# Performance work log

Measured on AMD Instinct MI355X. Metric: run time of the kernel, lower is better.

Reference implementation:

```python
import math
import jax, jax.numpy as jnp
import numpy as np

B, C, T, N, H = 4, 512, 2048, 4096, 4


def setup_inputs() -> dict:
    key = jax.random.key(0)
    ks = jax.random.split(key, 6)
    w = lambda k, shape: jax.random.normal(k, shape, dtype=jnp.float32) * 0.02
    return {
        "hidden_states": jax.random.normal(ks[0], (B, C, T), dtype=jnp.float32),
        "codebook_hidden_states": jax.random.normal(ks[1], (N, C), dtype=jnp.float32),
        # Linear weights stored as (in, out) so application is x @ W + b
        "Wq": w(ks[2], (C, C)), "bq": jnp.zeros((C,), jnp.float32),
        "Wk": w(ks[3], (C, C)), "bk": jnp.zeros((C,), jnp.float32),
        "Wv": w(ks[4], (C, C)), "bv": jnp.zeros((C,), jnp.float32),
        "Wp": w(ks[5], (C, H)), "bp": jnp.zeros((H,), jnp.float32),
    }


def reference(hidden_states, codebook_hidden_states, Wq, bq, Wk, bk, Wv, bv, Wp, bp):
    b, c, t = hidden_states.shape
    n = codebook_hidden_states.shape[0]
    h = bp.shape[0]
    d = c // h
    hs = hidden_states.transpose(0, 2, 1)                               # [B,T,C]
    q = (hs @ Wq + bq).reshape(b, t, h, d).transpose(0, 2, 1, 3)        # [B,H,T,d]
    k = (codebook_hidden_states @ Wk + bk).reshape(n, h, d).transpose(1, 0, 2)  # [H,N,d]
    v = codebook_hidden_states @ Wv + bv                                # [N,C]
    cg = hs @ Wp + bp                                                   # [B,T,H] head-pool gates
    scale = 1.0 / math.sqrt(d)
    logits_h = jnp.einsum('bhtd,hnd->bhnt', q, k) * scale               # [B,H,N,T]
    logits = jnp.einsum('bth,bhnt->bnt', cg, logits_h) / math.sqrt(h)   # [B,N,T]
    soft = jax.nn.softmax(logits, axis=1)                               # over codebook axis N
    idx = jnp.argmax(soft, axis=1)                                      # [B,T]
    hard = jax.nn.one_hot(idx, n, dtype=logits.dtype).transpose(0, 2, 1)  # [B,N,T]
    # straight-through: value == hard, gradient flows through soft
    one_hot = soft + jax.lax.stop_gradient(hard - soft)
    z_q = jnp.einsum('bnt,nd->bdt', one_hot, v)                         # [B,C,T]
    return logits, idx[:, None, :], z_q
```

## Files before the change

kernel.cpp:

```cpp
#include <hip/hip_runtime.h>
#include <hip/hip_bf16.h>
#include <cstddef>
#include <cstdint>

#define BB 4
#define CC 512
#define TT 2048
#define NN 4096
#define HH 4

constexpr float KFAC       = 0.04419417382415922f;
constexpr float INV_S18    = 1.0f / 262144.0f;
constexpr float INV_SCALE2 = 1.0f / (512.0f * 512.0f);

typedef _Float16 f16x8 __attribute__((ext_vector_type(8)));
typedef _Float16 f16x4 __attribute__((ext_vector_type(4)));
typedef float    f32x4 __attribute__((ext_vector_type(4)));

__device__ __forceinline__ void gld16(const void* g, void* s) {
    __builtin_amdgcn_global_load_lds(
        (const __attribute__((address_space(1))) void*)g,
        (__attribute__((address_space(3))) void*)s, 16, 0, 0);
}

struct HL { _Float16 h, l; };
__device__ __forceinline__ HL split512(float x) {
    float v = x * 512.0f;
    _Float16 h = (_Float16)v;
    return { h, (_Float16)(v - (float)h) };
}

__global__ __launch_bounds__(256) void k_split(
    const float* __restrict__ src, _Float16* __restrict__ hi, _Float16* __restrict__ lo, int n4)
{
    int q = blockIdx.x * 256 + threadIdx.x;
    if (q >= n4) return;
    float4 v = *(const float4*)(src + (size_t)q * 4);
    f16x4 H, L;
    HL a = split512(v.x); H[0] = a.h; L[0] = a.l;
    HL b = split512(v.y); H[1] = b.h; L[1] = b.l;
    HL c = split512(v.z); H[2] = c.h; L[2] = c.l;
    HL d = split512(v.w); H[3] = d.h; L[3] = d.l;
    *(f16x4*)(hi + (size_t)q * 4) = H;
    *(f16x4*)(lo + (size_t)q * 4) = L;
}

__device__ __forceinline__ void tsplit_body(
    const float* __restrict__ src, _Float16* __restrict__ hi, _Float16* __restrict__ lo,
    int S, int R, int r0, int s0)
{
    __shared__ float ls[64][65];
    const int tid = threadIdx.x;
    #pragma unroll
    for (int i = 0; i < 4; ++i) {
        int q = tid + i * 256;
        int row = q >> 4, c4 = (q & 15) * 4;
        float4 v = *(const float4*)(src + (size_t)(r0 + row) * S + s0 + c4);
        ls[row][c4] = v.x; ls[row][c4 + 1] = v.y;
        ls[row][c4 + 2] = v.z; ls[row][c4 + 3] = v.w;
    }
    __syncthreads();
    #pragma unroll
    for (int i = 0; i < 2; ++i) {
        int q = tid + i * 256;
        int orow = q >> 3, seg = (q & 7) * 8;
        f16x8 H, L;
        #pragma unroll
        for (int j = 0; j < 8; ++j) {
            HL s = split512(ls[seg + j][orow]);
            H[j] = s.h; L[j] = s.l;
        }
        size_t off = (size_t)(s0 + orow) * R + r0 + seg;
        *(f16x8*)(hi + off) = H;
        *(f16x8*)(lo + off) = L;
    }
}

__global__ __launch_bounds__(256) void k_tsplit(
    const float* __restrict__ src, _Float16* __restrict__ hi, _Float16* __restrict__ lo,
    long sbatch, long dbatch, int S, int R)
{
    src += (size_t)blockIdx.z * sbatch;
    hi  += (size_t)blockIdx.z * dbatch;
    lo  += (size_t)blockIdx.z * dbatch;
    tsplit_body(src, hi, lo, S, R, blockIdx.y * 64, blockIdx.x * 64);
}

__global__ __launch_bounds__(256) void k_tsplit_w(
    const float* __restrict__ w0, const float* __restrict__ w1, const float* __restrict__ w2,
    _Float16* __restrict__ h0, _Float16* __restrict__ h1, _Float16* __restrict__ h2,
    _Float16* __restrict__ l0, _Float16* __restrict__ l1, _Float16* __restrict__ l2)
{
    const int z = blockIdx.z;
    const float* src = z == 0 ? w0 : z == 1 ? w1 : w2;
    _Float16* hi = z == 0 ? h0 : z == 1 ? h1 : h2;
    _Float16* lo = z == 0 ? l0 : z == 1 ? l1 : l2;
    tsplit_body(src, hi, lo, CC, CC, blockIdx.y * 64, blockIdx.x * 64);
}

#define MFMA_TILE_DECLS                                                       \
    __shared__ __align__(16) _Float16 Ah[128][32];                            \
    __shared__ __align__(16) _Float16 Al[128][32];                            \
    __shared__ __align__(16) _Float16 Bh[128][32];                            \
    __shared__ __align__(16) _Float16 Bl[128][32];                            \
    const int tid  = threadIdx.x;                                             \
    const int w    = tid >> 6;                                                \
    const int l    = tid & 63;                                                \
    const int quad = l >> 4;                                                  \
    const int l15  = l & 15;                                                  \
    const int wm   = (w >> 1) * 64;                                           \
    const int wn   = (w & 1) * 64;                                            \
    const int rA   = l >> 2;                                                  \
    const int cA   = (l & 3) * 8;                                             \
    f32x4 acc[4][4];                                                          \
    _Pragma("unroll") for (int i = 0; i < 4; ++i)                             \
        _Pragma("unroll") for (int j = 0; j < 4; ++j)                         \
            acc[i][j] = (f32x4){0.f, 0.f, 0.f, 0.f};

#define MFMA_TILE_STAGE(pAh, pAl, pBh, pBl, k0, srcStride)                    \
    gld16(pAh + k0,                    &Ah[w * 32][0]);                       \
    gld16(pAh + k0 + 16 * (srcStride), &Ah[w * 32 + 16][0]);                  \
    gld16(pAl + k0,                    &Al[w * 32][0]);                       \
    gld16(pAl + k0 + 16 * (srcStride), &Al[w * 32 + 16][0]);                  \
    gld16(pBh + k0,                    &Bh[w * 32][0]);                       \
    gld16(pBh + k0 + 16 * (srcStride), &Bh[w * 32 + 16][0]);                  \
    gld16(pBl + k0,                    &Bl[w * 32][0]);                       \
    gld16(pBl + k0 + 16 * (srcStride), &Bl[w * 32 + 16][0]);

#define MFMA_TILE_COMPUTE                                                     \
    {                                                                         \
        f16x8 fah[4], fal[4], fbh[4], fbl[4];                                 \
        _Pragma("unroll") for (int i = 0; i < 4; ++i) {                       \
            fah[i] = *(const f16x8*)&Ah[wm + i * 16 + l15][quad * 8];         \
            fal[i] = *(const f16x8*)&Al[wm + i * 16 + l15][quad * 8];         \
            fbh[i] = *(const f16x8*)&Bh[wn + i * 16 + l15][quad * 8];         \
            fbl[i] = *(const f16x8*)&Bl[wn + i * 16 + l15][quad * 8];         \
        }                                                                     \
        _Pragma("unroll") for (int i = 0; i < 4; ++i)                         \
            _Pragma("unroll") for (int j = 0; j < 4; ++j) {                   \
                acc[i][j] = __builtin_amdgcn_mfma_f32_16x16x32_f16(fah[i], fbh[j], acc[i][j], 0, 0, 0); \
                acc[i][j] = __builtin_amdgcn_mfma_f32_16x16x32_f16(fah[i], fbl[j], acc[i][j], 0, 0, 0); \
                acc[i][j] = __builtin_amdgcn_mfma_f32_16x16x32_f16(fal[i], fbh[j], acc[i][j], 0, 0, 0); \
            }                                                                 \
    }

__global__ __launch_bounds__(256, 2) void k_proj_cb_mfma(
    const _Float16* __restrict__ cbhi, const _Float16* __restrict__ cblo,
    const _Float16* __restrict__ wkTh, const _Float16* __restrict__ wkTl,
    const _Float16* __restrict__ wvTh, const _Float16* __restrict__ wvTl,
    const float* __restrict__ bk, const float* __restrict__ bv,
    _Float16* __restrict__ khi, _Float16* __restrict__ klo, float* __restrict__ vproj)
{
    const int z  = blockIdx.z;
    const _Float16* bTh = z ? wvTh : wkTh;
    const _Float16* bTl = z ? wvTl : wkTl;
    const float* bias   = z ? bv : bk;
    const int m0 = blockIdx.y * 128;
    const int c0 = blockIdx.x * 128;

    MFMA_TILE_DECLS
    const _Float16* pAh = cbhi + (size_t)(m0 + w * 32 + rA) * CC + cA;
    const _Float16* pAl = cblo + (size_t)(m0 + w * 32 + rA) * CC + cA;
    const _Float16* pBh = bTh  + (size_t)(c0 + w * 32 + rA) * CC + cA;
    const _Float16* pBl = bTl  + (size_t)(c0 + w * 32 + rA) * CC + cA;

    for (int k0 = 0; k0 < CC; k0 += 32) {
        MFMA_TILE_STAGE(pAh, pAl, pBh, pBl, k0, CC)
        __syncthreads();
        MFMA_TILE_COMPUTE
        __syncthreads();
    }

    if (z == 0) {
        #pragma unroll
        for (int i = 0; i < 4; ++i)
            #pragma unroll
            for (int j = 0; j < 4; ++j) {
                int col = c0 + wn + j * 16 + l15;
                float bi = bias[col];
                #pragma unroll
                for (int r = 0; r < 4; ++r) {
                    int row = m0 + wm + i * 16 + quad * 4 + r;
                    float v = fmaf(acc[i][j][r], INV_S18, bi);
                    HL s = split512(v);
                    khi[(size_t)row * CC + col] = s.h;
                    klo[(size_t)row * CC + col] = s.l;
                }
            }
    } else {
        #pragma unroll
        for (int i = 0; i < 4; ++i)
            #pragma unroll
            for (int j = 0; j < 4; ++j) {
                int col = c0 + wn + j * 16 + l15;
                float bi = bias[col];
                #pragma unroll
                for (int r = 0; r < 4; ++r) {
                    int row = m0 + wm + i * 16 + quad * 4 + r;
                    vproj[(size_t)row * CC + col] = fmaf(acc[i][j][r], INV_S18, bi);
                }
            }
    }
}

__global__ __launch_bounds__(256, 2) void k_proj_q_mfma(
    const _Float16* __restrict__ ah_g, const _Float16* __restrict__ al_g,
    const _Float16* __restrict__ wqTh, const _Float16* __restrict__ wqTl,
    const float* __restrict__ bq, const float* __restrict__ Wp, const float* __restrict__ bp,
    _Float16* __restrict__ qhi, _Float16* __restrict__ qlo)
{
    const int m0   = blockIdx.y * 128;
    const int c0   = blockIdx.x * 128;
    const int hblk = c0 >> 7;

    MFMA_TILE_DECLS
    __shared__ float wp_sh[32];
    __shared__ float gate_sh[128];
    float gate = 0.f;

    const _Float16* pAh = ah_g + (size_t)(m0 + w * 32 + rA) * CC + cA;
    const _Float16* pAl = al_g + (size_t)(m0 + w * 32 + rA) * CC + cA;
    const _Float16* pBh = wqTh + (size_t)(c0 + w * 32 + rA) * CC + cA;
    const _Float16* pBl = wqTl + (size_t)(c0 + w * 32 + rA) * CC + cA;

    for (int k0 = 0; k0 < CC; k0 += 32) {
        MFMA_TILE_STAGE(pAh, pAl, pBh, pBl, k0, CC)
        if (tid < 32) wp_sh[tid] = Wp[(size_t)(k0 + tid) * HH + hblk];
        __syncthreads();
        MFMA_TILE_COMPUTE
        if (tid < 128) {
            #pragma unroll
            for (int s = 0; s < 4; ++s) {
                f16x8 hv = *(const f16x8*)&Ah[tid][s * 8];
                f16x8 lv = *(const f16x8*)&Al[tid][s * 8];
                #pragma unroll
                for (int jj = 0; jj < 8; ++jj)
                    gate = fmaf((float)hv[jj] + (float)lv[jj], wp_sh[s * 8 + jj], gate);
            }
        }
        __syncthreads();
    }
    if (tid < 128)
        gate_sh[tid] = (gate * (1.0f / 512.0f) + bp[hblk]) * KFAC;
    __syncthreads();

    #pragma unroll
    for (int i = 0; i < 4; ++i)
        #pragma unroll
        for (int j = 0; j < 4; ++j) {
            int col = c0 + wn + j * 16 + l15;
            float bi = bq[col];
            #pragma unroll
            for (int r = 0; r < 4; ++r) {
                int rloc = wm + i * 16 + quad * 4 + r;
                float v = fmaf(acc[i][j][r], INV_S18, bi) * gate_sh[rloc];
                HL s = split512(v);
                qhi[(size_t)(m0 + rloc) * CC + col] = s.h;
                qlo[(size_t)(m0 + rloc) * CC + col] = s.l;
            }
        }
}

__global__ __launch_bounds__(256, 2) void k_logits_mfma(
    const _Float16* __restrict__ khi, const _Float16* __restrict__ klo,
    const _Float16* __restrict__ qhi, const _Float16* __restrict__ qlo,
    float* __restrict__ logits)
{
    const int b  = blockIdx.z;
    const int t0 = blockIdx.x * 128;
    const int n0 = blockIdx.y * 128;

    MFMA_TILE_DECLS
    const _Float16* pAh = khi + (size_t)(n0 + w * 32 + rA) * CC + cA;
    const _Float16* pAl = klo + (size_t)(n0 + w * 32 + rA) * CC + cA;
    const _Float16* pBh = qhi + ((size_t)b * TT + t0 + w * 32 + rA) * CC + cA;
    const _Float16* pBl = qlo + ((size_t)b * TT + t0 + w * 32 + rA) * CC + cA;

    for (int k0 = 0; k0 < CC; k0 += 32) {
        MFMA_TILE_STAGE(pAh, pAl, pBh, pBl, k0, CC)
        __syncthreads();
        MFMA_TILE_COMPUTE
        __syncthreads();
    }

    #pragma unroll
    for (int i = 0; i < 4; ++i)
        #pragma unroll
        for (int j = 0; j < 4; ++j) {
            int col = t0 + wn + j * 16 + l15;
            #pragma unroll
            for (int r = 0; r < 4; ++r) {
                int row = n0 + wm + i * 16 + quad * 4 + r;
                logits[((size_t)b * NN + row) * TT + col] = acc[i][j][r] * INV_SCALE2;
            }
        }
}

__global__ __launch_bounds__(256) void k_argmax_gather(
    const float* __restrict__ logits,
    const float* __restrict__ vproj,
    float* __restrict__ idx_out,
    float* __restrict__ zq)
{
    const int b  = blockIdx.y;
    const int t0 = blockIdx.x * 32;
    const int tx = threadIdx.x & 31;
    const int ty = threadIdx.x >> 5;
    const float* base = logits + (size_t)b * NN * TT + t0 + tx;

    float best = -3.0e38f;
    int bi = ty * 512;
    #pragma unroll 4
    for (int n = ty * 512; n < ty * 512 + 512; ++n) {
        float v = base[(size_t)n * TT];
        if (v > best) { best = v; bi = n; }
    }

    __shared__ float sval[8][33];
    __shared__ int   sidx[8][33];
    __shared__ int   sfin[32];
    sval[ty][tx] = best;
    sidx[ty][tx] = bi;
    __syncthreads();
    if (ty == 0) {
        #pragma unroll
        for (int j = 1; j < 8; ++j) {
            float v = sval[j][tx];
            if (v > best) { best = v; bi = sidx[j][tx]; }
        }
        idx_out[(size_t)b * TT + t0 + tx] = (float)bi;
        sfin[tx] = bi;
    }
    __syncthreads();
    for (int pos = threadIdx.x; pos < 32 * CC; pos += 256) {
        int c = pos >> 5, tl = pos & 31;
        zq[((size_t)b * CC + c) * TT + t0 + tl] = vproj[(size_t)sfin[tl] * CC + c];
    }
}

extern "C" void kernel_launch(void* const* d_in, const int* in_sizes, int n_in,
                              void* d_out, int out_size, void* d_ws, size_t ws_size,
                              hipStream_t stream)
{
    (void)in_sizes; (void)n_in; (void)out_size; (void)ws_size;
    const float* hs = (const float*)d_in[0];
    const float* cb = (const float*)d_in[1];
    const float* Wq = (const float*)d_in[2];
    const float* bq = (const float*)d_in[3];
    const float* Wk = (const float*)d_in[4];
    const float* bk = (const float*)d_in[5];
    const float* Wv = (const float*)d_in[6];
    const float* bv = (const float*)d_in[7];
    const float* Wp = (const float*)d_in[8];
    const float* bp = (const float*)d_in[9];

    char* ws = (char*)d_ws;
    const size_t MB = 1024 * 1024;
    _Float16* hsTh = (_Float16*)(ws);
    _Float16* hsTl = (_Float16*)(ws + 8  * MB);
    _Float16* qhi  = (_Float16*)(ws + 16 * MB);
    _Float16* qlo  = (_Float16*)(ws + 24 * MB);
    _Float16* cbhi = (_Float16*)(ws + 32 * MB);
    _Float16* cblo = (_Float16*)(ws + 36 * MB);
    _Float16* khi  = (_Float16*)(ws + 40 * MB);
    _Float16* klo  = (_Float16*)(ws + 44 * MB);
    float*    vproj= (float*)   (ws + 48 * MB);
    _Float16* wqTh = (_Float16*)(ws + 56 * MB);
    _Float16* wqTl = (_Float16*)(ws + 56 * MB + 524288);
    _Float16* wkTh = (_Float16*)(ws + 57 * MB);
    _Float16* wkTl = (_Float16*)(ws + 57 * MB + 524288);
    _Float16* wvTh = (_Float16*)(ws + 58 * MB);
    _Float16* wvTl = (_Float16*)(ws + 58 * MB + 524288);

    float* logits = (float*)d_out;
    float* idxf   = logits + (size_t)BB * NN * TT;
    float* zq     = idxf + (size_t)BB * TT;

    k_split<<<dim3((NN * CC / 4 + 255) / 256), 256, 0, stream>>>(
        cb, cbhi, cblo, NN * CC / 4);
    k_tsplit<<<dim3(TT / 64, CC / 64, BB), 256, 0, stream>>>(
        hs, hsTh, hsTl, (long)CC * TT, (long)TT * CC, TT, CC);
    k_tsplit_w<<<dim3(CC / 64, CC / 64, 3), 256, 0, stream>>>(
        Wq, Wk, Wv, wqTh, wkTh, wvTh, wqTl, wkTl, wvTl);

    k_proj_cb_mfma<<<dim3(CC / 128, NN / 128, 2), 256, 0, stream>>>(
        cbhi, cblo, wkTh, wkTl, wvTh, wvTl, bk, bv, khi, klo, vproj);
    k_proj_q_mfma<<<dim3(CC / 128, (BB * TT) / 128), 256, 0, stream>>>(
        hsTh, hsTl, wqTh, wqTl, bq, Wp, bp, qhi, qlo);

    k_logits_mfma<<<dim3(TT / 128, NN / 128, BB), 256, 0, stream>>>(
        khi, klo, qhi, qlo, logits);

    k_argmax_gather<<<dim3(TT / 32, BB), 256, 0, stream>>>(
        logits, vproj, idxf, zq);
}
```

Measured before the change: 392.0 us.

## Fuse argmax partials into logits epilogue and merge projection launches

```diff
diff --git a/kernel.cpp b/kernel.cpp
--- a/kernel.cpp
+++ b/kernel.cpp
@@ -144,34 +144,78 @@
             }                                                                 \
     }
 
-__global__ __launch_bounds__(256, 2) void k_proj_cb_mfma(
+__global__ __launch_bounds__(256, 2) void k_proj_all(
+    const _Float16* __restrict__ hsTh, const _Float16* __restrict__ hsTl,
     const _Float16* __restrict__ cbhi, const _Float16* __restrict__ cblo,
+    const _Float16* __restrict__ wqTh, const _Float16* __restrict__ wqTl,
     const _Float16* __restrict__ wkTh, const _Float16* __restrict__ wkTl,
     const _Float16* __restrict__ wvTh, const _Float16* __restrict__ wvTl,
-    const float* __restrict__ bk, const float* __restrict__ bv,
+    const float* __restrict__ bq, const float* __restrict__ bk, const float* __restrict__ bv,
+    const float* __restrict__ Wp, const float* __restrict__ bp,
+    _Float16* __restrict__ qhi, _Float16* __restrict__ qlo,
     _Float16* __restrict__ khi, _Float16* __restrict__ klo, float* __restrict__ vproj)
 {
-    const int z  = blockIdx.z;
-    const _Float16* bTh = z ? wvTh : wkTh;
-    const _Float16* bTl = z ? wvTl : wkTl;
-    const float* bias   = z ? bv : bk;
-    const int m0 = blockIdx.y * 128;
-    const int c0 = blockIdx.x * 128;
+    const int z    = blockIdx.z;
+    const int y    = blockIdx.y;
+    const int c0   = blockIdx.x * 128;
+    const int path = z == 0 ? 0 : (y < 32 ? 1 : 2);
+    const int m0   = (z == 0 ? y : (y & 31)) * 128;
+    const int hblk = c0 >> 7;
+
+    const _Float16* srcAh = z == 0 ? hsTh : cbhi;
+    const _Float16* srcAl = z == 0 ? hsTl : cblo;
+    const _Float16* bTh   = path == 0 ? wqTh : path == 1 ? wkTh : wvTh;
+    const _Float16* bTl   = path == 0 ? wqTl : path == 1 ? wkTl : wvTl;
+    const float*    bias  = path == 0 ? bq   : path == 1 ? bk   : bv;
 
     MFMA_TILE_DECLS
-    const _Float16* pAh = cbhi + (size_t)(m0 + w * 32 + rA) * CC + cA;
-    const _Float16* pAl = cblo + (size_t)(m0 + w * 32 + rA) * CC + cA;
-    const _Float16* pBh = bTh  + (size_t)(c0 + w * 32 + rA) * CC + cA;
-    const _Float16* pBl = bTl  + (size_t)(c0 + w * 32 + rA) * CC + cA;
+    __shared__ float wp_sh[32];
+    __shared__ float gate_sh[128];
+    float gate = 0.f;
+
+    const _Float16* pAh = srcAh + (size_t)(m0 + w * 32 + rA) * CC + cA;
+    const _Float16* pAl = srcAl + (size_t)(m0 + w * 32 + rA) * CC + cA;
+    const _Float16* pBh = bTh   + (size_t)(c0 + w * 32 + rA) * CC + cA;
+    const _Float16* pBl = bTl   + (size_t)(c0 + w * 32 + rA) * CC + cA;
 
     for (int k0 = 0; k0 < CC; k0 += 32) {
         MFMA_TILE_STAGE(pAh, pAl, pBh, pBl, k0, CC)
+        if (path == 0 && tid < 32) wp_sh[tid] = Wp[(size_t)(k0 + tid) * HH + hblk];
         __syncthreads();
         MFMA_TILE_COMPUTE
+        if (path == 0 && tid < 128) {
+            #pragma unroll
+            for (int s = 0; s < 4; ++s) {
+                f16x8 hv = *(const f16x8*)&Ah[tid][s * 8];
+                f16x8 lv = *(const f16x8*)&Al[tid][s * 8];
+                #pragma unroll
+                for (int jj = 0; jj < 8; ++jj)
+                    gate = fmaf((float)hv[jj] + (float)lv[jj], wp_sh[s * 8 + jj], gate);
+            }
+        }
         __syncthreads();
     }
 
-    if (z == 0) {
+    if (path == 0) {
+        if (tid < 128)
+            gate_sh[tid] = (gate * (1.0f / 512.0f) + bp[hblk]) * KFAC;
+        __syncthreads();
+        #pragma unroll
+        for (int i = 0; i < 4; ++i)
+            #pragma unroll
+            for (int j = 0; j < 4; ++j) {
+                int col = c0 + wn + j * 16 + l15;
+                float bi = bias[col];
+                #pragma unroll
+                for (int r = 0; r < 4; ++r) {
+                    int rloc = wm + i * 16 + quad * 4 + r;
+                    float v = fmaf(acc[i][j][r], INV_S18, bi) * gate_sh[rloc];
+                    HL s = split512(v);
+                    qhi[(size_t)(m0 + rloc) * CC + col] = s.h;
+                    qlo[(size_t)(m0 + rloc) * CC + col] = s.l;
+                }
+            }
+    } else if (path == 1) {
         #pragma unroll
         for (int i = 0; i < 4; ++i)
             #pragma unroll
@@ -203,74 +247,21 @@
     }
 }
 
-__global__ __launch_bounds__(256, 2) void k_proj_q_mfma(
-    const _Float16* __restrict__ ah_g, const _Float16* __restrict__ al_g,
-    const _Float16* __restrict__ wqTh, const _Float16* __restrict__ wqTl,
-    const float* __restrict__ bq, const float* __restrict__ Wp, const float* __restrict__ bp,
-    _Float16* __restrict__ qhi, _Float16* __restrict__ qlo)
-{
-    const int m0   = blockIdx.y * 128;
-    const int c0   = blockIdx.x * 128;
-    const int hblk = c0 >> 7;
-
-    MFMA_TILE_DECLS
-    __shared__ float wp_sh[32];
-    __shared__ float gate_sh[128];
-    float gate = 0.f;
-
-    const _Float16* pAh = ah_g + (size_t)(m0 + w * 32 + rA) * CC + cA;
-    const _Float16* pAl = al_g + (size_t)(m0 + w * 32 + rA) * CC + cA;
-    const _Float16* pBh = wqTh + (size_t)(c0 + w * 32 + rA) * CC + cA;
-    const _Float16* pBl = wqTl + (size_t)(c0 + w * 32 + rA) * CC + cA;
-
-    for (int k0 = 0; k0 < CC; k0 += 32) {
-        MFMA_TILE_STAGE(pAh, pAl, pBh, pBl, k0, CC)
-        if (tid < 32) wp_sh[tid] = Wp[(size_t)(k0 + tid) * HH + hblk];
-        __syncthreads();
-        MFMA_TILE_COMPUTE
-        if (tid < 128) {
-            #pragma unroll
-            for (int s = 0; s < 4; ++s) {
-                f16x8 hv = *(const f16x8*)&Ah[tid][s * 8];
-                f16x8 lv = *(const f16x8*)&Al[tid][s * 8];
-                #pragma unroll
-                for (int jj = 0; jj < 8; ++jj)
-                    gate = fmaf((float)hv[jj] + (float)lv[jj], wp_sh[s * 8 + jj], gate);
-            }
-        }
-        __syncthreads();
-    }
-    if (tid < 128)
-        gate_sh[tid] = (gate * (1.0f / 512.0f) + bp[hblk]) * KFAC;
-    __syncthreads();
-
-    #pragma unroll
-    for (int i = 0; i < 4; ++i)
-        #pragma unroll
-        for (int j = 0; j < 4; ++j) {
-            int col = c0 + wn + j * 16 + l15;
-            float bi = bq[col];
-            #pragma unroll
-            for (int r = 0; r < 4; ++r) {
-                int rloc = wm + i * 16 + quad * 4 + r;
-                float v = fmaf(acc[i][j][r], INV_S18, bi) * gate_sh[rloc];
-                HL s = split512(v);
-                qhi[(size_t)(m0 + rloc) * CC + col] = s.h;
-                qlo[(size_t)(m0 + rloc) * CC + col] = s.l;
-            }
-        }
-}
-
 __global__ __launch_bounds__(256, 2) void k_logits_mfma(
     const _Float16* __restrict__ khi, const _Float16* __restrict__ klo,
     const _Float16* __restrict__ qhi, const _Float16* __restrict__ qlo,
-    float* __restrict__ logits)
+    float* __restrict__ logits,
+    float* __restrict__ pval,
+    int*   __restrict__ pidx)
 {
     const int b  = blockIdx.z;
     const int t0 = blockIdx.x * 128;
     const int n0 = blockIdx.y * 128;
 
     MFMA_TILE_DECLS
+    __shared__ float rval[128];
+    __shared__ int   ridx[128];
+
     const _Float16* pAh = khi + (size_t)(n0 + w * 32 + rA) * CC + cA;
     const _Float16* pAl = klo + (size_t)(n0 + w * 32 + rA) * CC + cA;
     const _Float16* pBh = qhi + ((size_t)b * TT + t0 + w * 32 + rA) * CC + cA;
@@ -283,56 +274,77 @@
         __syncthreads();
     }
 
+    float bvj[4]; int bnj[4];
     #pragma unroll
-    for (int i = 0; i < 4; ++i)
-        #pragma unroll
-        for (int j = 0; j < 4; ++j) {
-            int col = t0 + wn + j * 16 + l15;
+    for (int j = 0; j < 4; ++j) {
+        int col = t0 + wn + j * 16 + l15;
+        float bv = -3.0e38f; int bn = 0;
+        #pragma unroll
+        for (int i = 0; i < 4; ++i) {
             #pragma unroll
             for (int r = 0; r < 4; ++r) {
                 int row = n0 + wm + i * 16 + quad * 4 + r;
-                logits[((size_t)b * NN + row) * TT + col] = acc[i][j][r] * INV_SCALE2;
+                float v = acc[i][j][r] * INV_SCALE2;
+                logits[((size_t)b * NN + row) * TT + col] = v;
+                if (v > bv) { bv = v; bn = row; }
             }
         }
-}
-
-__global__ __launch_bounds__(256) void k_argmax_gather(
-    const float* __restrict__ logits,
+        #pragma unroll
+        for (int m = 16; m <= 32; m <<= 1) {
+            float ov = __shfl_xor(bv, m, 64);
+            int   on = __shfl_xor(bn, m, 64);
+            if (ov > bv || (ov == bv && on < bn)) { bv = ov; bn = on; }
+        }
+        bvj[j] = bv; bnj[j] = bn;
+    }
+    if (w >= 2 && l < 16) {
+        #pragma unroll
+        for (int j = 0; j < 4; ++j) {
+            rval[wn + j * 16 + l] = bvj[j];
+            ridx[wn + j * 16 + l] = bnj[j];
+        }
+    }
+    __syncthreads();
+    if (w < 2 && l < 16) {
+        #pragma unroll
+        for (int j = 0; j < 4; ++j) {
+            int cl = wn + j * 16 + l;
+            float bv = bvj[j]; int bn = bnj[j];
+            float ov = rval[cl];
+            if (ov > bv) { bv = ov; bn = ridx[cl]; }
+            size_t o = ((size_t)b * 32 + (n0 >> 7)) * TT + t0 + cl;
+            pval[o] = bv;
+            pidx[o] = bn;
+        }
+    }
+}
+
+__global__ __launch_bounds__(256) void k_finalize(
+    const float* __restrict__ pval,
+    const int*   __restrict__ pidx,
     const float* __restrict__ vproj,
     float* __restrict__ idx_out,
     float* __restrict__ zq)
 {
     const int b  = blockIdx.y;
     const int t0 = blockIdx.x * 32;
-    const int tx = threadIdx.x & 31;
-    const int ty = threadIdx.x >> 5;
-    const float* base = logits + (size_t)b * NN * TT + t0 + tx;
-
-    float best = -3.0e38f;
-    int bi = ty * 512;
-    #pragma unroll 4
-    for (int n = ty * 512; n < ty * 512 + 512; ++n) {
-        float v = base[(size_t)n * TT];
-        if (v > best) { best = v; bi = n; }
-    }
-
-    __shared__ float sval[8][33];
-    __shared__ int   sidx[8][33];
-    __shared__ int   sfin[32];
-    sval[ty][tx] = best;
-    sidx[ty][tx] = bi;
+    const int tid = threadIdx.x;
+
+    __shared__ int sfin[32];
+    if (tid < 32) {
+        const int t = t0 + tid;
+        float bv = -3.0e38f; int bn = 0;
+        #pragma unroll
+        for (int k = 0; k < 32; ++k) {
+            size_t o = ((size_t)b * 32 + k) * TT + t;
+            float v = pval[o];
+            if (v > bv) { bv = v; bn = pidx[o]; }
+        }
+        idx_out[(size_t)b * TT + t] = (float)bn;
+        sfin[tid] = bn;
+    }
     __syncthreads();
-    if (ty == 0) {
-        #pragma unroll
-        for (int j = 1; j < 8; ++j) {
-            float v = sval[j][tx];
-            if (v > best) { best = v; bi = sidx[j][tx]; }
-        }
-        idx_out[(size_t)b * TT + t0 + tx] = (float)bi;
-        sfin[tx] = bi;
-    }
-    __syncthreads();
-    for (int pos = threadIdx.x; pos < 32 * CC; pos += 256) {
+    for (int pos = tid; pos < 32 * CC; pos += 256) {
         int c = pos >> 5, tl = pos & 31;
         zq[((size_t)b * CC + c) * TT + t0 + tl] = vproj[(size_t)sfin[tl] * CC + c];
     }
@@ -371,6 +383,8 @@
     _Float16* wkTl = (_Float16*)(ws + 57 * MB + 524288);
     _Float16* wvTh = (_Float16*)(ws + 58 * MB);
     _Float16* wvTl = (_Float16*)(ws + 58 * MB + 524288);
+    float* pval = (float*)(ws + 32 * MB);
+    int*   pidx = (int*)  (ws + 33 * MB);
 
     float* logits = (float*)d_out;
     float* idxf   = logits + (size_t)BB * NN * TT;
@@ -383,14 +397,15 @@
     k_tsplit_w<<<dim3(CC / 64, CC / 64, 3), 256, 0, stream>>>(
         Wq, Wk, Wv, wqTh, wkTh, wvTh, wqTl, wkTl, wvTl);
 
-    k_proj_cb_mfma<<<dim3(CC / 128, NN / 128, 2), 256, 0, stream>>>(
-        cbhi, cblo, wkTh, wkTl, wvTh, wvTl, bk, bv, khi, klo, vproj);
-    k_proj_q_mfma<<<dim3(CC / 128, (BB * TT) / 128), 256, 0, stream>>>(
-        hsTh, hsTl, wqTh, wqTl, bq, Wp, bp, qhi, qlo);
+    k_proj_all<<<dim3(CC / 128, 64, 2), 256, 0, stream>>>(
+        hsTh, hsTl, cbhi, cblo,
+        wqTh, wqTl, wkTh, wkTl, wvTh, wvTl,
+        bq, bk, bv, Wp, bp,
+        qhi, qlo, khi, klo, vproj);
 
     k_logits_mfma<<<dim3(TT / 128, NN / 128, BB), 256, 0, stream>>>(
-        khi, klo, qhi, qlo, logits);
-
-    k_argmax_gather<<<dim3(TT / 32, BB), 256, 0, stream>>>(
-        logits, vproj, idxf, zq);
-}
+        khi, klo, qhi, qlo, logits, pval, pidx);
+
+    k_finalize<<<dim3(TT / 32, BB), 256, 0, stream>>>(
+        pval, pidx, vproj, idxf, zq);
+}
```

Result: faster. 336.7 us (-14.1%).
